# Kernel tuning notes

Hardware: AMD Instinct MI355X
Metric: run time of the kernel (lower is better)

## Reference

```python
import jax, jax.numpy as jnp
import numpy as np

N_NODES = 100000
N_EDGES = 300000
D_IN = 256
D_OUT = 256


def setup_inputs() -> dict:
    key = jax.random.key(0)
    k1, k2, k3 = jax.random.split(key, 3)
    z = jax.random.normal(k1, (N_NODES, D_IN), dtype=jnp.float32)
    edge_index = jax.random.randint(k2, (2, N_EDGES), 0, N_NODES, dtype=jnp.int64)
    # Linear(input_dim, out_dim): weight [out, in], stored transposed for x @ W
    W = jax.random.normal(k3, (D_IN, D_OUT), dtype=jnp.float32) / np.sqrt(D_IN)
    b = jnp.zeros((D_OUT,), dtype=jnp.float32)
    return {"z": z, "edge_index": edge_index, "W": W, "b": b}


def reference(z, edge_index, W, b):
    # h = Linear(z): [N, D_out]
    h = z @ W + b
    # gather endpoint embeddings and take per-edge dot product
    src = h[edge_index[0]]  # [E, D_out]
    dst = h[edge_index[1]]  # [E, D_out]
    value = jnp.sum(src * dst, axis=1)  # [E]
    return jax.nn.sigmoid(value)
```

## Files before the change

kernel.cpp:

```cpp
#include <hip/hip_runtime.h>
#include <hip/hip_bf16.h>
#include <hip/hip_fp16.h>
#include <math.h>


#define D_DIM 256
#define BM 128

typedef __attribute__((ext_vector_type(8))) _Float16 half8;
typedef __attribute__((ext_vector_type(4))) float f32x4;

__device__ half8 g_Wf[8 * 256 * 4];

__global__ __launch_bounds__(256) void pack_w_kernel(const float* __restrict__ W) {
  int t = blockIdx.x * 256 + threadIdx.x;
  int kb = t >> 10;
  int qd = (t >> 8) & 3;
  int n  = t & 255;
  half8 o;
#pragma unroll
  for (int j = 0; j < 8; j++)
    o[j] = (_Float16)W[(size_t)(kb * 32 + qd * 8 + j) * D_DIM + n];
  g_Wf[(kb * 256 + n) * 4 + qd] = o;
}

__device__ inline void stage_b(int kb, char* buf, int wv, int lane) {
  const char* gsrc = (const char*)g_Wf + (size_t)kb * 16384 + wv * 2048;
  char* ldst = buf + wv * 2048;
#pragma unroll
  for (int i = 0; i < 2; i++) {
    __builtin_amdgcn_global_load_lds(
        (const __attribute__((address_space(1))) void*)(gsrc + i * 1024 + lane * 16),
        (__attribute__((address_space(3))) void*)(ldst + i * 1024),
        16, 0, 0);
  }
}

__global__ __launch_bounds__(512) void gemm_mfma_kernel(
    const float* __restrict__ z, const float* __restrict__ b,
    __half* __restrict__ h, int nrows) {
  __shared__ char smem[34816];
  const int tid = threadIdx.x;
  const int lane = tid & 63;
  const int wv = tid >> 6;
  const int mg = wv >> 1;
  const int nh = wv & 1;
  const int fr = lane & 15;
  const int qd = lane >> 4;
  const int row0 = blockIdx.x * BM + mg * 32;

  f32x4 acc[2][8];
#pragma unroll
  for (int i = 0; i < 2; i++)
#pragma unroll
    for (int j = 0; j < 8; j++) acc[i][j] = (f32x4)0.f;

  const float* zrow[2];
#pragma unroll
  for (int fm = 0; fm < 2; fm++) {
    int r = row0 + fm * 16 + fr;
    r = r < nrows ? r : (nrows - 1);
    zrow[fm] = z + (size_t)r * D_DIM + qd * 8;
  }

  float4 a0[2], a1[2];
#pragma unroll
  for (int fm = 0; fm < 2; fm++) {
    a0[fm] = *(const float4*)(zrow[fm]);
    a1[fm] = *(const float4*)(zrow[fm] + 4);
  }
  stage_b(0, smem, wv, lane);
  __syncthreads();

#pragma unroll 1
  for (int kb = 0; kb < 8; kb++) {
    char* cur = smem + (kb & 1) * 16384;
    if (kb < 7) stage_b(kb + 1, smem + ((kb + 1) & 1) * 16384, wv, lane);

    half8 af[2];
#pragma unroll
    for (int fm = 0; fm < 2; fm++) {
      af[fm][0] = (_Float16)a0[fm].x; af[fm][1] = (_Float16)a0[fm].y;
      af[fm][2] = (_Float16)a0[fm].z; af[fm][3] = (_Float16)a0[fm].w;
      af[fm][4] = (_Float16)a1[fm].x; af[fm][5] = (_Float16)a1[fm].y;
      af[fm][6] = (_Float16)a1[fm].z; af[fm][7] = (_Float16)a1[fm].w;
    }
    if (kb < 7) {
#pragma unroll
      for (int fm = 0; fm < 2; fm++) {
        const float* p = zrow[fm] + (kb + 1) * 32;
        a0[fm] = *(const float4*)(p);
        a1[fm] = *(const float4*)(p + 4);
      }
    }

    const half8* buf = (const half8*)cur;
#pragma unroll
    for (int fn = 0; fn < 8; fn++) {
      int fi = (nh * 128 + fn * 16 + fr) * 4 + qd;
      half8 bf = buf[fi];
#pragma unroll
      for (int fm = 0; fm < 2; fm++)
        acc[fm][fn] = __builtin_amdgcn_mfma_f32_16x16x32_f16(af[fm], bf, acc[fm][fn], 0, 0, 0);
    }
    __syncthreads();
  }

  __half* et = (__half*)(smem + wv * 4352);
  float bias[8];
#pragma unroll
  for (int fn = 0; fn < 8; fn++) bias[fn] = b[nh * 128 + fn * 16 + fr];

#pragma unroll
  for (int fm = 0; fm < 2; fm++) {
#pragma unroll
    for (int fn = 0; fn < 8; fn++)
#pragma unroll
      for (int r = 0; r < 4; r++)
        et[(qd * 4 + r) * 136 + fn * 16 + fr] = __float2half(acc[fm][fn][r] + bias[fn]);
#pragma unroll
    for (int p = 0; p < 4; p++) {
      int idx = p * 64 + lane;
      int rr = idx >> 4;
      int cc = idx & 15;
      float4 v = *(const float4*)(et + rr * 136 + cc * 8);
      int row = row0 + fm * 16 + rr;
      if (row < nrows)
        *(float4*)(h + (size_t)row * D_DIM + nh * 128 + cc * 8) = v;
    }
  }
}

__global__ __launch_bounds__(256) void edge_dot_kernel(
    const int* __restrict__ ei, const __half* __restrict__ h,
    float* __restrict__ out, int E) {
  int wid = (blockIdx.x * blockDim.x + threadIdx.x) >> 6;
  int lane = threadIdx.x & 63;
  int ebase = wid * 8;
  if (ebase >= E) return;
  const int half = lane >> 5;
  const int off = lane & 31;

  float4 v[8];
#pragma unroll
  for (int q = 0; q < 8; q++) {
    int e = ebase + q;
    e = e < E ? e : (E - 1);
    int node = half ? ei[E + e] : ei[e];
    v[q] = *(const float4*)((const __half*)h + (size_t)node * D_DIM + off * 8);
  }

  float res = 0.f;
#pragma unroll
  for (int q = 0; q < 8; q++) {
    float4 w;
    w.x = __shfl_xor(v[q].x, 32);
    w.y = __shfl_xor(v[q].y, 32);
    w.z = __shfl_xor(v[q].z, 32);
    w.w = __shfl_xor(v[q].w, 32);
    const __half2* a2 = (const __half2*)&v[q];
    const __half2* b2 = (const __half2*)&w;
    float part = 0.f;
#pragma unroll
    for (int j = 0; j < 4; j++) {
      float2 fa = __half22float2(a2[j]);
      float2 fb = __half22float2(b2[j]);
      part += fa.x * fb.x + fa.y * fb.y;
    }
#pragma unroll
    for (int m = 1; m <= 16; m <<= 1) part += __shfl_xor(part, m);
    res = (lane == q) ? part : res;
  }
  if (lane < 8) {
    int e = ebase + lane;
    if (e < E) out[e] = 1.0f / (1.0f + __expf(-res));
  }
}

extern "C" void kernel_launch(void* const* d_in, const int* in_sizes, int n_in,
                              void* d_out, int out_size, void* d_ws, size_t ws_size,
                              hipStream_t stream) {
  const float* z  = (const float*)d_in[0];
  const int*   ei = (const int*)d_in[1];
  const float* W  = (const float*)d_in[2];
  const float* b  = (const float*)d_in[3];
  float* out = (float*)d_out;
  __half* h  = (__half*)d_ws;

  const int nnodes = in_sizes[0] / D_DIM;
  const int E = in_sizes[1] / 2;

  pack_w_kernel<<<32, 256, 0, stream>>>(W);

  dim3 grid_gemm((nnodes + BM - 1) / BM);
  gemm_mfma_kernel<<<grid_gemm, 512, 0, stream>>>(z, b, h, nnodes);

  int waves = (E + 7) / 8;
  dim3 grid_edge(((size_t)waves * 64 + 255) / 256);
  edge_dot_kernel<<<grid_edge, 256, 0, stream>>>(ei, h, out, E);
}
```

Baseline: 215.2 us.

## Load packed W directly into registers, drop LDS staging, halve GEMM block

```diff
diff --git a/kernel.cpp b/kernel.cpp
--- a/kernel.cpp
+++ b/kernel.cpp
@@ -5,7 +5,7 @@
 
 
 #define D_DIM 256
-#define BM 128
+#define BM 64
 
 typedef __attribute__((ext_vector_type(8))) _Float16 half8;
 typedef __attribute__((ext_vector_type(4))) float f32x4;
@@ -24,22 +24,10 @@
   g_Wf[(kb * 256 + n) * 4 + qd] = o;
 }
 
-__device__ inline void stage_b(int kb, char* buf, int wv, int lane) {
-  const char* gsrc = (const char*)g_Wf + (size_t)kb * 16384 + wv * 2048;
-  char* ldst = buf + wv * 2048;
-#pragma unroll
-  for (int i = 0; i < 2; i++) {
-    __builtin_amdgcn_global_load_lds(
-        (const __attribute__((address_space(1))) void*)(gsrc + i * 1024 + lane * 16),
-        (__attribute__((address_space(3))) void*)(ldst + i * 1024),
-        16, 0, 0);
-  }
-}
-
-__global__ __launch_bounds__(512) void gemm_mfma_kernel(
+__global__ __launch_bounds__(256) void gemm_mfma_kernel(
     const float* __restrict__ z, const float* __restrict__ b,
     __half* __restrict__ h, int nrows) {
-  __shared__ char smem[34816];
+  __shared__ char smem[4 * 4352];
   const int tid = threadIdx.x;
   const int lane = tid & 63;
   const int wv = tid >> 6;
@@ -63,47 +51,58 @@
     zrow[fm] = z + (size_t)r * D_DIM + qd * 8;
   }
 
-  float4 a0[2], a1[2];
-#pragma unroll
-  for (int fm = 0; fm < 2; fm++) {
-    a0[fm] = *(const float4*)(zrow[fm]);
-    a1[fm] = *(const float4*)(zrow[fm] + 4);
-  }
-  stage_b(0, smem, wv, lane);
-  __syncthreads();
-
-#pragma unroll 1
+  const half8* gw = g_Wf;
+  const int bbase = ((nh * 128 + fr) << 2) + qd;
+
+  float4 a0[3][2], a1[3][2];
+  half8 bf[2][8];
+
+#pragma unroll
+  for (int s = 0; s < 2; s++)
+#pragma unroll
+    for (int fm = 0; fm < 2; fm++) {
+      const float* p = zrow[fm] + s * 32;
+      a0[s][fm] = *(const float4*)(p);
+      a1[s][fm] = *(const float4*)(p + 4);
+    }
+#pragma unroll
+  for (int fn = 0; fn < 8; fn++) bf[0][fn] = gw[fn * 64 + bbase];
+
+#pragma unroll
   for (int kb = 0; kb < 8; kb++) {
-    char* cur = smem + (kb & 1) * 16384;
-    if (kb < 7) stage_b(kb + 1, smem + ((kb + 1) & 1) * 16384, wv, lane);
+    const int cA = kb % 3;
+    const int pA = (kb + 2) % 3;
+    const int cB = kb & 1;
+    const int nB = cB ^ 1;
+
+    if (kb < 6) {
+#pragma unroll
+      for (int fm = 0; fm < 2; fm++) {
+        const float* p = zrow[fm] + (kb + 2) * 32;
+        a0[pA][fm] = *(const float4*)(p);
+        a1[pA][fm] = *(const float4*)(p + 4);
+      }
+    }
+    if (kb < 7) {
+#pragma unroll
+      for (int fn = 0; fn < 8; fn++)
+        bf[nB][fn] = gw[(kb + 1) * 1024 + fn * 64 + bbase];
+    }
 
     half8 af[2];
 #pragma unroll
     for (int fm = 0; fm < 2; fm++) {
-      af[fm][0] = (_Float16)a0[fm].x; af[fm][1] = (_Float16)a0[fm].y;
-      af[fm][2] = (_Float16)a0[fm].z; af[fm][3] = (_Float16)a0[fm].w;
-      af[fm][4] = (_Float16)a1[fm].x; af[fm][5] = (_Float16)a1[fm].y;
-      af[fm][6] = (_Float16)a1[fm].z; af[fm][7] = (_Float16)a1[fm].w;
-    }
-    if (kb < 7) {
-#pragma unroll
-      for (int fm = 0; fm < 2; fm++) {
-        const float* p = zrow[fm] + (kb + 1) * 32;
-        a0[fm] = *(const float4*)(p);
-        a1[fm] = *(const float4*)(p + 4);
-      }
-    }
-
-    const half8* buf = (const half8*)cur;
-#pragma unroll
-    for (int fn = 0; fn < 8; fn++) {
-      int fi = (nh * 128 + fn * 16 + fr) * 4 + qd;
-      half8 bf = buf[fi];
+      af[fm][0] = (_Float16)a0[cA][fm].x; af[fm][1] = (_Float16)a0[cA][fm].y;
+      af[fm][2] = (_Float16)a0[cA][fm].z; af[fm][3] = (_Float16)a0[cA][fm].w;
+      af[fm][4] = (_Float16)a1[cA][fm].x; af[fm][5] = (_Float16)a1[cA][fm].y;
+      af[fm][6] = (_Float16)a1[cA][fm].z; af[fm][7] = (_Float16)a1[cA][fm].w;
+    }
+
+#pragma unroll
+    for (int fn = 0; fn < 8; fn++)
 #pragma unroll
       for (int fm = 0; fm < 2; fm++)
-        acc[fm][fn] = __builtin_amdgcn_mfma_f32_16x16x32_f16(af[fm], bf, acc[fm][fn], 0, 0, 0);
-    }
-    __syncthreads();
+        acc[fm][fn] = __builtin_amdgcn_mfma_f32_16x16x32_f16(af[fm], bf[cB][fn], acc[fm][fn], 0, 0, 0);
   }
 
   __half* et = (__half*)(smem + wv * 4352);
@@ -193,7 +192,7 @@
   pack_w_kernel<<<32, 256, 0, stream>>>(W);
 
   dim3 grid_gemm((nnodes + BM - 1) / BM);
-  gemm_mfma_kernel<<<grid_gemm, 512, 0, stream>>>(z, b, h, nnodes);
+  gemm_mfma_kernel<<<grid_gemm, 256, 0, stream>>>(z, b, h, nnodes);
 
   int waves = (E + 7) / 8;
   dim3 grid_edge(((size_t)waves * 64 + 255) / 256);
```

New measurement: 230.6 us. 1.07x slower.

## Pipeline GEMM A loads with register double-buffering and partial vmcnt barriers

Applied to the files above, without the earlier changes.

```diff
diff --git a/kernel.cpp b/kernel.cpp
--- a/kernel.cpp
+++ b/kernel.cpp
@@ -36,7 +36,7 @@
   }
 }
 
-__global__ __launch_bounds__(512) void gemm_mfma_kernel(
+__global__ __launch_bounds__(512, 4) void gemm_mfma_kernel(
     const float* __restrict__ z, const float* __restrict__ b,
     __half* __restrict__ h, int nrows) {
   __shared__ char smem[34816];
@@ -63,35 +63,42 @@
     zrow[fm] = z + (size_t)r * D_DIM + qd * 8;
   }
 
-  float4 a0[2], a1[2];
+  float4 a0[2][2], a1[2][2];
+
+  stage_b(0, smem, wv, lane);
+  asm volatile("" ::: "memory");
 #pragma unroll
   for (int fm = 0; fm < 2; fm++) {
-    a0[fm] = *(const float4*)(zrow[fm]);
-    a1[fm] = *(const float4*)(zrow[fm] + 4);
-  }
-  stage_b(0, smem, wv, lane);
-  __syncthreads();
-
-#pragma unroll 1
+    a0[0][fm] = *(const float4*)(zrow[fm]);
+    a1[0][fm] = *(const float4*)(zrow[fm] + 4);
+  }
+  asm volatile("s_waitcnt vmcnt(4)" ::: "memory");
+  __builtin_amdgcn_s_barrier();
+
+#pragma unroll
   for (int kb = 0; kb < 8; kb++) {
+    const int cA = kb & 1;
+    const int nA = cA ^ 1;
     char* cur = smem + (kb & 1) * 16384;
-    if (kb < 7) stage_b(kb + 1, smem + ((kb + 1) & 1) * 16384, wv, lane);
-
-    half8 af[2];
-#pragma unroll
-    for (int fm = 0; fm < 2; fm++) {
-      af[fm][0] = (_Float16)a0[fm].x; af[fm][1] = (_Float16)a0[fm].y;
-      af[fm][2] = (_Float16)a0[fm].z; af[fm][3] = (_Float16)a0[fm].w;
-      af[fm][4] = (_Float16)a1[fm].x; af[fm][5] = (_Float16)a1[fm].y;
-      af[fm][6] = (_Float16)a1[fm].z; af[fm][7] = (_Float16)a1[fm].w;
-    }
+
     if (kb < 7) {
+      stage_b(kb + 1, smem + ((kb + 1) & 1) * 16384, wv, lane);
+      asm volatile("" ::: "memory");
 #pragma unroll
       for (int fm = 0; fm < 2; fm++) {
         const float* p = zrow[fm] + (kb + 1) * 32;
-        a0[fm] = *(const float4*)(p);
-        a1[fm] = *(const float4*)(p + 4);
+        a0[nA][fm] = *(const float4*)(p);
+        a1[nA][fm] = *(const float4*)(p + 4);
       }
+    }
+
+    half8 af[2];
+#pragma unroll
+    for (int fm = 0; fm < 2; fm++) {
+      af[fm][0] = (_Float16)a0[cA][fm].x; af[fm][1] = (_Float16)a0[cA][fm].y;
+      af[fm][2] = (_Float16)a0[cA][fm].z; af[fm][3] = (_Float16)a0[cA][fm].w;
+      af[fm][4] = (_Float16)a1[cA][fm].x; af[fm][5] = (_Float16)a1[cA][fm].y;
+      af[fm][6] = (_Float16)a1[cA][fm].z; af[fm][7] = (_Float16)a1[cA][fm].w;
     }
 
     const half8* buf = (const half8*)cur;
@@ -103,7 +110,10 @@
       for (int fm = 0; fm < 2; fm++)
         acc[fm][fn] = __builtin_amdgcn_mfma_f32_16x16x32_f16(af[fm], bf, acc[fm][fn], 0, 0, 0);
     }
-    __syncthreads();
+
+    if (kb < 7) asm volatile("s_waitcnt vmcnt(4)" ::: "memory");
+    else        asm volatile("s_waitcnt vmcnt(0)" ::: "memory");
+    __builtin_amdgcn_s_barrier();
   }
 
   __half* et = (__half*)(smem + wv * 4352);
```

Result: slower. 219.7 us (+2.1%).
